# Optimization experiments

Hardware: AMD Instinct MI355X
Metric: run time of the kernel (lower is better)

The kernel has to match this reference:

```python
import jax, jax.numpy as jnp
import numpy as np

# ---- model hyperparameters (match init_kwargs) ----
NUM_INPUT, NUM_HIDDEN, NUM_OUTPUT = 2048, 65536, 512
FAN_OUT = 256
TAU, THRESHOLD = 20.0, 0.3
SPIKE_DELAY = 1  # must be 1 for the one-step-delay scan formulation below
N = NUM_INPUT + NUM_HIDDEN + NUM_OUTPUT
HID_START, OUT_START = NUM_INPUT, NUM_INPUT + NUM_HIDDEN
SURROGATE_SCALE = 25.0


@jax.custom_vjp
def spike(v):
    """Heaviside spike with sigmoid surrogate gradient (SurrogateSpike)."""
    return (v >= THRESHOLD).astype(v.dtype)

def _spike_fwd(v):
    return spike(v), v

def _spike_bwd(v, g):
    s = jax.nn.sigmoid(SURROGATE_SCALE * (v - THRESHOLD))
    return (g * SURROGATE_SCALE * s * (1.0 - s),)

spike.defvjp(_spike_fwd, _spike_bwd)


def make_targets(seed=42):
    """Structured random connectivity (mirrors _generate_random_targets ranges)."""
    rng = np.random.default_rng(seed)
    t = np.empty((N, FAN_OUT), dtype=np.int64)
    # input neurons -> hidden
    t[:NUM_INPUT] = rng.integers(HID_START, OUT_START, size=(NUM_INPUT, FAN_OUT))
    # hidden neurons -> hidden+output, excluding self
    hid = rng.integers(HID_START, N, size=(NUM_HIDDEN, FAN_OUT))
    src = np.arange(HID_START, OUT_START)[:, None]
    R = N - HID_START
    hid = np.where(hid == src, HID_START + (hid - HID_START + 1) % R, hid)
    t[HID_START:OUT_START] = hid
    # output neurons -> hidden
    t[OUT_START:] = rng.integers(HID_START, OUT_START, size=(NUM_OUTPUT, FAN_OUT))
    return jnp.asarray(t, dtype=jnp.int32)


def setup_inputs() -> dict:
    key = jax.random.key(0)
    k1, k2 = jax.random.split(key)
    weights = jax.random.normal(k1, (N, FAN_OUT), dtype=jnp.float32) * 0.3
    input_spikes = jax.random.bernoulli(k2, 0.2, (NUM_INPUT,))
    return {"input_spikes": input_spikes, "weights": weights,
            "targets": make_targets(), "max_timesteps": 50}


def _simulate(input_spikes, weights, targets, max_timesteps):
    decay_base = jnp.exp(jnp.float32(-1.0 / TAU))
    idx = jnp.arange(N)
    flat_targets = targets.reshape(-1)  # [N*FAN_OUT]

    inp = jnp.zeros(N, bool).at[:NUM_INPUT].set(input_spikes)
    pot = jnp.zeros(N, jnp.float32)
    last_update = jnp.zeros(N, jnp.int32)
    has_fired = inp
    strength = jnp.where(inp, 2.0, 0.0).astype(jnp.float32)
    out_times = jnp.full(NUM_OUTPUT, -1, jnp.int32)
    fire_now = inp  # input spikes scheduled on the wheel at t=0

    def step(carry, t):
        pot, last_update, has_fired, strength, fire_now, out_times = carry
        # contributions of spiking sources: spike_strength[src] * weights[src]
        src_val = jnp.where(fire_now, strength, 0.0)                 # [N]
        contrib = (src_val[:, None] * weights).reshape(-1)           # [N*FAN_OUT]
        # neurons that receive at least one spike this step (the 'unique_targets')
        hits = jnp.zeros(N, jnp.float32).at[flat_targets].add(
            jnp.repeat(fire_now.astype(jnp.float32), FAN_OUT))
        is_target = hits > 0
        # lazy retroactive decay only on touched neurons
        dt = (t - last_update).astype(jnp.float32)
        pot = jnp.where(is_target, pot * decay_base ** dt, pot)
        last_update = jnp.where(is_target, t, last_update)
        # scatter-add contributions (zeros for non-firing sources)
        pot = pot.at[flat_targets].add(contrib)
        # spike check with refractory mask
        probs = spike(pot) * (1.0 - has_fired.astype(jnp.float32))
        new_fired = probs > 0.5
        has_fired = has_fired | new_fired
        strength = jnp.where(new_fired, probs, strength)
        out_times = jnp.where(new_fired[OUT_START:] & (out_times < 0), t, out_times)
        # schedule hidden spikes for delivery at t + 1 (spike_delay == 1)
        fire_next = new_fired & (idx < OUT_START)
        # reset membrane of newly fired non-output neurons
        reset = jnp.where(idx >= OUT_START, 0.0, probs)
        pot = pot * (1.0 - reset)
        return (pot, last_update, has_fired, strength, fire_next, out_times), None

    carry = (pot, last_update, has_fired, strength, fire_now, out_times)
    carry, _ = jax.lax.scan(step, carry, jnp.arange(max_timesteps, dtype=jnp.int32))
    pot, last_update, has_fired, strength, _, out_times = carry
    # final decay to end of simulation window
    final_dt = (max_timesteps - last_update).astype(jnp.float32)
    pot = pot * decay_base ** final_dt
    return out_times, pot[OUT_START:]


def reference(input_spikes, weights, targets, max_timesteps):
    out_times, out_pot = _simulate(input_spikes, weights, targets, max_timesteps)
    return out_times, out_pot
```

## Files before the change

kernel.cpp:

```cpp
#include <hip/hip_runtime.h>
#include <math.h>

#define N_TOTAL    68096
#define NUM_INPUT  2048
#define NUM_OUTPUT 512
#define OUT_START  67584
#define N_TGT      66048
#define FAN_OUT    256
#define THRESH     0.3f
#define T_MAX      50
#define T_BIG      12
#define BM_WORDS   2064
#define LIST_CAP   12288

#define HALF_SZ    33024
#define N_CHUNK    128
#define DENSE_THR  2000

__device__ __forceinline__ int calc_chunks(int fcnt) {
    int c = fcnt >> 7;
    if (c < 1) c = 1;
    if (c > N_CHUNK) c = N_CHUNK;
    return c;
}

__global__ __launch_bounds__(256) void init_k(
    const unsigned int* __restrict__ in0,
    float* pot, float* acc, int* last_up, unsigned char* fired,
    int* frontier0, int* cnt, float* out_f, float* decay_tab)
{
    __shared__ int sF, sG;
    const int tid = threadIdx.x;
    if (tid == 0) { sF = 0; sG = 0; }
    __syncthreads();
    for (int k = tid; k < 512; k += 256) {
        unsigned int v = in0[k];
        if (v == 0x3F800000u) atomicAdd(&sF, 1);
        else if (v > 1u)      sG = 1;
    }
    __syncthreads();
    const int mode = (sF >= 8) ? 1 : (sG ? 2 : 0);

    const int i = blockIdx.x * 256 + tid;
    const int lane = tid & 63;
    if (i <= T_MAX) {
        float base = expf(-0.05f);
        decay_tab[i] = (float)pow((double)base, (double)i);
    }
    if (i < NUM_OUTPUT) out_f[i] = -1.0f;
    bool want = false;
    if (i < N_TOTAL) {
        pot[i] = 0.0f;
        acc[i] = 0.0f;
        last_up[i] = 0;
        bool s = false;
        if (i < NUM_INPUT) {
            if (mode == 0)      s = ((const int*)in0)[i] != 0;
            else if (mode == 1) s = ((const float*)in0)[i] != 0.0f;
            else                s = ((const unsigned char*)in0)[i] != 0;
        }
        fired[i] = s ? 1 : 0;
        want = s;
    }
    unsigned long long m = __ballot(want);
    if (m) {
        int leader = __ffsll((long long)m) - 1;
        int base = 0;
        if (lane == leader) base = atomicAdd(&cnt[0], __popcll(m));
        base = __shfl(base, leader, 64);
        if (want) {
            int off = __popcll(m & ((1ull << (unsigned)lane) - 1ull));
            frontier0[base + off] = i;
        }
    }
}

__global__ __launch_bounds__(1024) void step_scatter_k(
    const int* __restrict__ fr, const int* __restrict__ cnt_cur,
    int* cnt_next,
    const int* __restrict__ targets, const float* __restrict__ weights,
    float* __restrict__ acc, float* __restrict__ rep)
{
    __shared__ float lacc[HALF_SZ];
    const int fcnt = *cnt_cur;
    const int tid  = threadIdx.x;
    if (blockIdx.x == 0 && tid == 0) *cnt_next = 0;
    if (fcnt == 0) return;

    if (fcnt < DENSE_THR) {
        const int nq = fcnt * (FAN_OUT / 4);
        const int stride = gridDim.x * 1024;
        for (int q = blockIdx.x * 1024 + tid; q < nq; q += stride) {
            int s  = fr[q >> 6];
            int j4 = (q & 63) << 2;
            const int base = s * FAN_OUT + j4;
            int4   tg = *(const int4*)  (targets + base);
            float4 wv = *(const float4*)(weights + base);
            float  st = (s < NUM_INPUT) ? 2.0f : 1.0f;
            atomicAdd(&acc[tg.x], st * wv.x);
            atomicAdd(&acc[tg.y], st * wv.y);
            atomicAdd(&acc[tg.z], st * wv.z);
            atomicAdd(&acc[tg.w], st * wv.w);
        }
        return;
    }

    const int chunks = calc_chunks(fcnt);
    const int c = blockIdx.x & 127;
    const int h = blockIdx.x >> 7;
    if (c >= chunks) return;
    const int base = NUM_INPUT + h * HALF_SZ;
    for (int k = tid; k < HALF_SZ / 4; k += 1024)
        ((float4*)lacc)[k] = make_float4(0.f, 0.f, 0.f, 0.f);
    __syncthreads();
    const int lo = (int)(((long long)fcnt * c)       / chunks);
    const int hi = (int)(((long long)fcnt * (c + 1)) / chunks);
    const int nq = (hi - lo) << 6;
    for (int q = tid; q < nq; q += 2048) {
        const int q2 = q + 1024;
        const bool hasB = q2 < nq;
        const int sA  = fr[lo + (q >> 6)];
        const int sB  = hasB ? fr[lo + (q2 >> 6)] : sA;
        const int ebA = sA * FAN_OUT + ((q  & 63) << 2);
        const int ebB = sB * FAN_OUT + ((q2 & 63) << 2);
        int4   tgA = *(const int4*)  (targets + ebA);
        float4 wvA = *(const float4*)(weights + ebA);
        int4   tgB = *(const int4*)  (targets + ebB);
        float4 wvB = *(const float4*)(weights + ebB);
        const float stA = (sA < NUM_INPUT) ? 2.0f : 1.0f;
        const float stB = (sB < NUM_INPUT) ? 2.0f : 1.0f;
        int x;
        x = tgA.x - base; if ((unsigned)x < HALF_SZ) atomicAdd(&lacc[x], stA * wvA.x);
        x = tgA.y - base; if ((unsigned)x < HALF_SZ) atomicAdd(&lacc[x], stA * wvA.y);
        x = tgA.z - base; if ((unsigned)x < HALF_SZ) atomicAdd(&lacc[x], stA * wvA.z);
        x = tgA.w - base; if ((unsigned)x < HALF_SZ) atomicAdd(&lacc[x], stA * wvA.w);
        if (hasB) {
            x = tgB.x - base; if ((unsigned)x < HALF_SZ) atomicAdd(&lacc[x], stB * wvB.x);
            x = tgB.y - base; if ((unsigned)x < HALF_SZ) atomicAdd(&lacc[x], stB * wvB.y);
            x = tgB.z - base; if ((unsigned)x < HALF_SZ) atomicAdd(&lacc[x], stB * wvB.z);
            x = tgB.w - base; if ((unsigned)x < HALF_SZ) atomicAdd(&lacc[x], stB * wvB.w);
        }
    }
    __syncthreads();
    float4* out = (float4*)(rep + (size_t)((c << 1) + h) * HALF_SZ);
    for (int k = tid; k < HALF_SZ / 4; k += 1024) out[k] = ((float4*)lacc)[k];
}

__global__ __launch_bounds__(128) void step_update_k(
    const float* __restrict__ rep, const int* __restrict__ cnt_cur,
    float* __restrict__ pot, float* __restrict__ acc,
    int* __restrict__ last_up, unsigned char* __restrict__ fired,
    int* __restrict__ frontier_next, int* __restrict__ cnt_next,
    float* __restrict__ out_f, const float* __restrict__ decay_tab, int t)
{
    const int fcnt = *cnt_cur;
    if (fcnt == 0) return;
    const int g = blockIdx.x * 128 + threadIdx.x;
    const int lane = threadIdx.x & 63;
    bool w2 = false;
    const int n = NUM_INPUT + g;
    {
        float a;
        if (fcnt < DENSE_THR) {
            a = acc[n];
            if (a != 0.0f) acc[n] = 0.0f;
        } else {
            const int chunks = calc_chunks(fcnt);
            const int hh  = (g >= HALF_SZ) ? 1 : 0;
            const int idx = g - hh * HALF_SZ;
            const float* p0 = rep + (size_t)hh * HALF_SZ + idx;
            float a0 = 0.f, a1 = 0.f, a2 = 0.f, a3 = 0.f;
            int c = 0;
            for (; c + 3 < chunks; c += 4) {
                a0 += p0[(size_t)((c + 0) << 1) * HALF_SZ];
                a1 += p0[(size_t)((c + 1) << 1) * HALF_SZ];
                a2 += p0[(size_t)((c + 2) << 1) * HALF_SZ];
                a3 += p0[(size_t)((c + 3) << 1) * HALF_SZ];
            }
            for (; c < chunks; ++c)
                a0 += p0[(size_t)(c << 1) * HALF_SZ];
            a = (a0 + a1) + (a2 + a3);
        }
        if (a != 0.0f) {
            float p = pot[n] * decay_tab[t - last_up[n]] + a;
            last_up[n] = t;
            if (!fired[n] && p >= THRESH) {
                fired[n] = 1;
                if (n < OUT_START) { p = 0.0f; w2 = true; }
                else out_f[n - OUT_START] = (float)t;
            }
            pot[n] = p;
        }
    }
    unsigned long long m = __ballot(w2);
    if (m) {
        int leader = __ffsll((long long)m) - 1;
        int base = 0;
        if (lane == leader) base = atomicAdd(cnt_next, __popcll(m));
        base = __shfl(base, leader, 64);
        if (w2) {
            int off = __popcll(m & ((1ull << (unsigned)lane) - 1ull));
            frontier_next[base + off] = n;
        }
    }
}

__global__ __launch_bounds__(1024) void tail_k(
    float* __restrict__ pot, float* __restrict__ acc,
    int* __restrict__ last_up, unsigned char* __restrict__ fired,
    int* __restrict__ fr0, int* __restrict__ fr1, int* __restrict__ cnt,
    const int* __restrict__ targets, const float* __restrict__ weights,
    float* __restrict__ out_f, const float* __restrict__ decay_tab)
{
    __shared__ unsigned bm[BM_WORDS];
    __shared__ int      lst[LIST_CAP];
    __shared__ int      lcnt, ovf;
    __shared__ float    sdecay[T_MAX + 1];
    const int tid = threadIdx.x;
    if (tid <= T_MAX) sdecay[tid] = decay_tab[tid];

    for (int t = T_BIG; t < T_MAX; ++t) {
        const int cur = t & 1, nxt = cur ^ 1;
        for (int k = tid; k < BM_WORDS; k += 1024) bm[k] = 0u;
        if (tid == 0) { lcnt = 0; ovf = 0; cnt[nxt] = 0; }
        __syncthreads();
        const int fcnt = cnt[cur];
        if (fcnt == 0) break;
        const int* fr  = (cur == 0) ? fr0 : fr1;
        int*       frn = (cur == 0) ? fr1 : fr0;

        const int nq = fcnt * (FAN_OUT / 4);
        for (int q = tid; q < nq; q += 1024) {
            int s  = fr[q >> 6];
            int j4 = (q & 63) << 2;
            const int base = s * FAN_OUT + j4;
            int4   tg = *(const int4*)  (targets + base);
            float4 wv = *(const float4*)(weights + base);
            float  st = (s < NUM_INPUT) ? 2.0f : 1.0f;
            #define EDGE(TG, WV) do {                                         \
                atomicAdd(&acc[TG], st * (WV));                               \
                int b = (TG) - NUM_INPUT;                                     \
                unsigned bit = 1u << (b & 31);                                \
                unsigned old = atomicOr(&bm[b >> 5], bit);                    \
                if (!(old & bit)) {                                           \
                    int p_ = atomicAdd(&lcnt, 1);                             \
                    if (p_ < LIST_CAP) lst[p_] = (TG); else ovf = 1;          \
                } } while (0)
            EDGE(tg.x, wv.x); EDGE(tg.y, wv.y);
            EDGE(tg.z, wv.z); EDGE(tg.w, wv.w);
            #undef EDGE
        }
        __syncthreads();

        const int M = lcnt;
        const bool full = (ovf != 0);
        const int lo = full ? (NUM_INPUT + tid) : tid;
        const int hi = full ? N_TOTAL : M;
        for (int k = lo; k < hi; k += 1024) {
            const int n = full ? k : lst[k];
            float a = __hip_atomic_load(&acc[n], __ATOMIC_RELAXED,
                                        __HIP_MEMORY_SCOPE_AGENT);
            if (a != 0.0f) {
                __hip_atomic_store(&acc[n], 0.0f, __ATOMIC_RELAXED,
                                   __HIP_MEMORY_SCOPE_AGENT);
                float p = pot[n] * sdecay[t - last_up[n]] + a;
                last_up[n] = t;
                if (!fired[n] && p >= THRESH) {
                    fired[n] = 1;
                    if (n < OUT_START) {
                        p = 0.0f;
                        int pos = atomicAdd(&cnt[nxt], 1);
                        frn[pos] = n;
                    } else out_f[n - OUT_START] = (float)t;
                }
                pot[n] = p;
            }
        }
        __syncthreads();
    }

    __syncthreads();
    for (int i = tid; i < NUM_OUTPUT; i += 1024) {
        int n = OUT_START + i;
        out_f[NUM_OUTPUT + i] = pot[n] * sdecay[T_MAX - last_up[n]];
    }
}

extern "C" void kernel_launch(void* const* d_in, const int* in_sizes, int n_in,
                              void* d_out, int out_size, void* d_ws, size_t ws_size,
                              hipStream_t stream) {
    const void*  in_spikes = d_in[0];
    const float* weights   = (const float*)d_in[1];
    const int*   targets   = (const int*)d_in[2];
    float*       out_f     = (float*)d_out;

    char* w = (char*)d_ws;
    int*   cnt       = (int*)w;
    float* decay_tab = (float*)(w + 256);
    float* pot       = (float*)(w + 512);
    float* acc       = pot + N_TOTAL;
    int*   last_up   = (int*)(acc + N_TOTAL);
    int*   fr0       = last_up + N_TOTAL;
    int*   fr1       = fr0 + N_TOTAL;
    unsigned char* fired = (unsigned char*)(fr1 + N_TOTAL);
    size_t base_bytes = (size_t)((char*)(fired + N_TOTAL) - w);
    size_t rep_off    = (base_bytes + 255) & ~(size_t)255;
    float* rep        = (float*)(w + rep_off);

    hipMemsetAsync(cnt, 0, 16, stream);
    init_k<<<266, 256, 0, stream>>>((const unsigned int*)in_spikes,
                                    pot, acc, last_up, fired,
                                    fr0, cnt, out_f, decay_tab);

    int* fr[2] = {fr0, fr1};
    for (int t = 0; t < T_BIG; ++t) {
        const int cur = t & 1, nxt = cur ^ 1;
        step_scatter_k<<<2 * N_CHUNK, 1024, 0, stream>>>(
            fr[cur], &cnt[cur], &cnt[nxt], targets, weights, acc, rep);
        step_update_k<<<516, 128, 0, stream>>>(
            rep, &cnt[cur], pot, acc, last_up, fired,
            fr[nxt], &cnt[nxt], out_f, decay_tab, t);
    }
    tail_k<<<1, 1024, 0, stream>>>(pot, acc, last_up, fired, fr0, fr1, cnt,
                                   targets, weights, out_f, decay_tab);
}
```

Baseline: 320.5 us.

## Skip scatter to already-fired hidden neurons via shared fired bitmask

Keeps a global bitmask of hidden neurons that have already fired and copies it into shared memory in the scatter kernels. Edges whose target already fired are dropped, and the weight load is skipped when all four targets in a vector are dead. The update kernels skip already-fired neurons. It also raises the dense threshold so more steps take the global-atomic path. The trade-offs are extra shared memory and bitmask reads, and the pot/last_up values of fired hidden neurons no longer change, which only matters if those values are observed.

```diff
diff --git a/kernel.cpp b/kernel.cpp
--- a/kernel.cpp
+++ b/kernel.cpp
@@ -6,6 +6,8 @@
 #define NUM_OUTPUT 512
 #define OUT_START  67584
 #define N_TGT      66048
+#define NUM_HIDDEN 65536
+#define FB_WORDS   2048
 #define FAN_OUT    256
 #define THRESH     0.3f
 #define T_MAX      50
@@ -15,7 +17,8 @@
 
 #define HALF_SZ    33024
 #define N_CHUNK    128
-#define DENSE_THR  2000
+#define DENSE_THR  6000
+
 
 __device__ __forceinline__ int calc_chunks(int fcnt) {
     int c = fcnt >> 7;
@@ -27,7 +30,8 @@
 __global__ __launch_bounds__(256) void init_k(
     const unsigned int* __restrict__ in0,
     float* pot, float* acc, int* last_up, unsigned char* fired,
-    int* frontier0, int* cnt, float* out_f, float* decay_tab)
+    int* frontier0, int* cnt, float* out_f, float* decay_tab,
+    unsigned* fbits)
 {
     __shared__ int sF, sG;
     const int tid = threadIdx.x;
@@ -48,6 +52,7 @@
         decay_tab[i] = (float)pow((double)base, (double)i);
     }
     if (i < NUM_OUTPUT) out_f[i] = -1.0f;
+    if (i < FB_WORDS)   fbits[i] = 0u;
     bool want = false;
     if (i < N_TOTAL) {
         pot[i] = 0.0f;
@@ -75,32 +80,44 @@
     }
 }
 
+#define LIVE(SFB, TG) ({ int b_ = (TG) - NUM_INPUT; \
+    (b_ >= NUM_HIDDEN) || !((SFB[b_ >> 5] >> (b_ & 31)) & 1u); })
+
 __global__ __launch_bounds__(1024) void step_scatter_k(
     const int* __restrict__ fr, const int* __restrict__ cnt_cur,
     int* cnt_next,
     const int* __restrict__ targets, const float* __restrict__ weights,
-    float* __restrict__ acc, float* __restrict__ rep)
+    float* __restrict__ acc, float* __restrict__ rep,
+    const unsigned* __restrict__ fbits)
 {
-    __shared__ float lacc[HALF_SZ];
+    __shared__ float    lacc[HALF_SZ];
+    __shared__ unsigned sfb[FB_WORDS];
     const int fcnt = *cnt_cur;
     const int tid  = threadIdx.x;
     if (blockIdx.x == 0 && tid == 0) *cnt_next = 0;
     if (fcnt == 0) return;
 
+    for (int k = tid; k < FB_WORDS; k += 1024) sfb[k] = fbits[k];
+
     if (fcnt < DENSE_THR) {
+        __syncthreads();
         const int nq = fcnt * (FAN_OUT / 4);
         const int stride = gridDim.x * 1024;
         for (int q = blockIdx.x * 1024 + tid; q < nq; q += stride) {
             int s  = fr[q >> 6];
             int j4 = (q & 63) << 2;
             const int base = s * FAN_OUT + j4;
-            int4   tg = *(const int4*)  (targets + base);
-            float4 wv = *(const float4*)(weights + base);
-            float  st = (s < NUM_INPUT) ? 2.0f : 1.0f;
-            atomicAdd(&acc[tg.x], st * wv.x);
-            atomicAdd(&acc[tg.y], st * wv.y);
-            atomicAdd(&acc[tg.z], st * wv.z);
-            atomicAdd(&acc[tg.w], st * wv.w);
+            int4 tg = *(const int4*)(targets + base);
+            const bool lx = LIVE(sfb, tg.x), ly = LIVE(sfb, tg.y);
+            const bool lz = LIVE(sfb, tg.z), lw = LIVE(sfb, tg.w);
+            if (lx | ly | lz | lw) {
+                float4 wv = *(const float4*)(weights + base);
+                float  st = (s < NUM_INPUT) ? 2.0f : 1.0f;
+                if (lx) atomicAdd(&acc[tg.x], st * wv.x);
+                if (ly) atomicAdd(&acc[tg.y], st * wv.y);
+                if (lz) atomicAdd(&acc[tg.z], st * wv.z);
+                if (lw) atomicAdd(&acc[tg.w], st * wv.w);
+            }
         }
         return;
     }
@@ -123,22 +140,36 @@
         const int sB  = hasB ? fr[lo + (q2 >> 6)] : sA;
         const int ebA = sA * FAN_OUT + ((q  & 63) << 2);
         const int ebB = sB * FAN_OUT + ((q2 & 63) << 2);
-        int4   tgA = *(const int4*)  (targets + ebA);
-        float4 wvA = *(const float4*)(weights + ebA);
-        int4   tgB = *(const int4*)  (targets + ebB);
-        float4 wvB = *(const float4*)(weights + ebB);
-        const float stA = (sA < NUM_INPUT) ? 2.0f : 1.0f;
-        const float stB = (sB < NUM_INPUT) ? 2.0f : 1.0f;
+        int4 tgA = *(const int4*)(targets + ebA);
+        int4 tgB = *(const int4*)(targets + ebB);
         int x;
-        x = tgA.x - base; if ((unsigned)x < HALF_SZ) atomicAdd(&lacc[x], stA * wvA.x);
-        x = tgA.y - base; if ((unsigned)x < HALF_SZ) atomicAdd(&lacc[x], stA * wvA.y);
-        x = tgA.z - base; if ((unsigned)x < HALF_SZ) atomicAdd(&lacc[x], stA * wvA.z);
-        x = tgA.w - base; if ((unsigned)x < HALF_SZ) atomicAdd(&lacc[x], stA * wvA.w);
+        {
+            x = tgA.x - base; const bool kx = (unsigned)x < HALF_SZ && LIVE(sfb, tgA.x);
+            int y = tgA.y - base; const bool ky = (unsigned)y < HALF_SZ && LIVE(sfb, tgA.y);
+            int z = tgA.z - base; const bool kz = (unsigned)z < HALF_SZ && LIVE(sfb, tgA.z);
+            int u = tgA.w - base; const bool ku = (unsigned)u < HALF_SZ && LIVE(sfb, tgA.w);
+            if (kx | ky | kz | ku) {
+                float4 wv = *(const float4*)(weights + ebA);
+                const float st = (sA < NUM_INPUT) ? 2.0f : 1.0f;
+                if (kx) atomicAdd(&lacc[x], st * wv.x);
+                if (ky) atomicAdd(&lacc[y], st * wv.y);
+                if (kz) atomicAdd(&lacc[z], st * wv.z);
+                if (ku) atomicAdd(&lacc[u], st * wv.w);
+            }
+        }
         if (hasB) {
-            x = tgB.x - base; if ((unsigned)x < HALF_SZ) atomicAdd(&lacc[x], stB * wvB.x);
-            x = tgB.y - base; if ((unsigned)x < HALF_SZ) atomicAdd(&lacc[x], stB * wvB.y);
-            x = tgB.z - base; if ((unsigned)x < HALF_SZ) atomicAdd(&lacc[x], stB * wvB.z);
-            x = tgB.w - base; if ((unsigned)x < HALF_SZ) atomicAdd(&lacc[x], stB * wvB.w);
+            x = tgB.x - base; const bool kx = (unsigned)x < HALF_SZ && LIVE(sfb, tgB.x);
+            int y = tgB.y - base; const bool ky = (unsigned)y < HALF_SZ && LIVE(sfb, tgB.y);
+            int z = tgB.z - base; const bool kz = (unsigned)z < HALF_SZ && LIVE(sfb, tgB.z);
+            int u = tgB.w - base; const bool ku = (unsigned)u < HALF_SZ && LIVE(sfb, tgB.w);
+            if (kx | ky | kz | ku) {
+                float4 wv = *(const float4*)(weights + ebB);
+                const float st = (sB < NUM_INPUT) ? 2.0f : 1.0f;
+                if (kx) atomicAdd(&lacc[x], st * wv.x);
+                if (ky) atomicAdd(&lacc[y], st * wv.y);
+                if (kz) atomicAdd(&lacc[z], st * wv.z);
+                if (ku) atomicAdd(&lacc[u], st * wv.w);
+            }
         }
     }
     __syncthreads();
@@ -151,7 +182,8 @@
     float* __restrict__ pot, float* __restrict__ acc,
     int* __restrict__ last_up, unsigned char* __restrict__ fired,
     int* __restrict__ frontier_next, int* __restrict__ cnt_next,
-    float* __restrict__ out_f, const float* __restrict__ decay_tab, int t)
+    float* __restrict__ out_f, const float* __restrict__ decay_tab, int t,
+    unsigned* __restrict__ fbits)
 {
     const int fcnt = *cnt_cur;
     if (fcnt == 0) return;
@@ -159,7 +191,7 @@
     const int lane = threadIdx.x & 63;
     bool w2 = false;
     const int n = NUM_INPUT + g;
-    {
+    if (n >= OUT_START || !fired[n]) {
         float a;
         if (fcnt < DENSE_THR) {
             a = acc[n];
@@ -186,8 +218,11 @@
             last_up[n] = t;
             if (!fired[n] && p >= THRESH) {
                 fired[n] = 1;
-                if (n < OUT_START) { p = 0.0f; w2 = true; }
-                else out_f[n - OUT_START] = (float)t;
+                if (n < OUT_START) {
+                    p = 0.0f; w2 = true;
+                    const int b = n - NUM_INPUT;
+                    atomicOr(&fbits[b >> 5], 1u << (b & 31));
+                } else out_f[n - OUT_START] = (float)t;
             }
             pot[n] = p;
         }
@@ -210,14 +245,17 @@
     int* __restrict__ last_up, unsigned char* __restrict__ fired,
     int* __restrict__ fr0, int* __restrict__ fr1, int* __restrict__ cnt,
     const int* __restrict__ targets, const float* __restrict__ weights,
-    float* __restrict__ out_f, const float* __restrict__ decay_tab)
+    float* __restrict__ out_f, const float* __restrict__ decay_tab,
+    const unsigned* __restrict__ fbits)
 {
     __shared__ unsigned bm[BM_WORDS];
+    __shared__ unsigned sfb[FB_WORDS];
     __shared__ int      lst[LIST_CAP];
     __shared__ int      lcnt, ovf;
     __shared__ float    sdecay[T_MAX + 1];
     const int tid = threadIdx.x;
     if (tid <= T_MAX) sdecay[tid] = decay_tab[tid];
+    for (int k = tid; k < FB_WORDS; k += 1024) sfb[k] = fbits[k];
 
     for (int t = T_BIG; t < T_MAX; ++t) {
         const int cur = t & 1, nxt = cur ^ 1;
@@ -234,10 +272,13 @@
             int s  = fr[q >> 6];
             int j4 = (q & 63) << 2;
             const int base = s * FAN_OUT + j4;
-            int4   tg = *(const int4*)  (targets + base);
+            int4 tg = *(const int4*)(targets + base);
+            const bool lx = LIVE(sfb, tg.x), ly = LIVE(sfb, tg.y);
+            const bool lz = LIVE(sfb, tg.z), lw = LIVE(sfb, tg.w);
+            if (!(lx | ly | lz | lw)) continue;
             float4 wv = *(const float4*)(weights + base);
             float  st = (s < NUM_INPUT) ? 2.0f : 1.0f;
-            #define EDGE(TG, WV) do {                                         \
+            #define EDGE(L, TG, WV) if (L) {                                  \
                 atomicAdd(&acc[TG], st * (WV));                               \
                 int b = (TG) - NUM_INPUT;                                     \
                 unsigned bit = 1u << (b & 31);                                \
@@ -245,9 +286,9 @@
                 if (!(old & bit)) {                                           \
                     int p_ = atomicAdd(&lcnt, 1);                             \
                     if (p_ < LIST_CAP) lst[p_] = (TG); else ovf = 1;          \
-                } } while (0)
-            EDGE(tg.x, wv.x); EDGE(tg.y, wv.y);
-            EDGE(tg.z, wv.z); EDGE(tg.w, wv.w);
+                } }
+            EDGE(lx, tg.x, wv.x); EDGE(ly, tg.y, wv.y);
+            EDGE(lz, tg.z, wv.z); EDGE(lw, tg.w, wv.w);
             #undef EDGE
         }
         __syncthreads();
@@ -258,6 +299,7 @@
         const int hi = full ? N_TOTAL : M;
         for (int k = lo; k < hi; k += 1024) {
             const int n = full ? k : lst[k];
+            if (n < OUT_START && fired[n]) continue;
             float a = __hip_atomic_load(&acc[n], __ATOMIC_RELAXED,
                                         __HIP_MEMORY_SCOPE_AGENT);
             if (a != 0.0f) {
@@ -271,6 +313,8 @@
                         p = 0.0f;
                         int pos = atomicAdd(&cnt[nxt], 1);
                         frn[pos] = n;
+                        const int b = n - NUM_INPUT;
+                        atomicOr(&sfb[b >> 5], 1u << (b & 31));
                     } else out_f[n - OUT_START] = (float)t;
                 }
                 pot[n] = p;
@@ -295,14 +339,15 @@
     float*       out_f     = (float*)d_out;
 
     char* w = (char*)d_ws;
-    int*   cnt       = (int*)w;
-    float* decay_tab = (float*)(w + 256);
-    float* pot       = (float*)(w + 512);
-    float* acc       = pot + N_TOTAL;
-    int*   last_up   = (int*)(acc + N_TOTAL);
-    int*   fr0       = last_up + N_TOTAL;
-    int*   fr1       = fr0 + N_TOTAL;
-    unsigned char* fired = (unsigned char*)(fr1 + N_TOTAL);
+    int*      cnt       = (int*)w;
+    float*    decay_tab = (float*)(w + 256);
+    float*    pot       = (float*)(w + 512);
+    float*    acc       = pot + N_TOTAL;
+    int*      last_up   = (int*)(acc + N_TOTAL);
+    int*      fr0       = last_up + N_TOTAL;
+    int*      fr1       = fr0 + N_TOTAL;
+    unsigned* fbits     = (unsigned*)(fr1 + N_TOTAL);
+    unsigned char* fired = (unsigned char*)(fbits + FB_WORDS);
     size_t base_bytes = (size_t)((char*)(fired + N_TOTAL) - w);
     size_t rep_off    = (base_bytes + 255) & ~(size_t)255;
     float* rep        = (float*)(w + rep_off);
@@ -310,17 +355,17 @@
     hipMemsetAsync(cnt, 0, 16, stream);
     init_k<<<266, 256, 0, stream>>>((const unsigned int*)in_spikes,
                                     pot, acc, last_up, fired,
-                                    fr0, cnt, out_f, decay_tab);
+                                    fr0, cnt, out_f, decay_tab, fbits);
 
     int* fr[2] = {fr0, fr1};
     for (int t = 0; t < T_BIG; ++t) {
         const int cur = t & 1, nxt = cur ^ 1;
         step_scatter_k<<<2 * N_CHUNK, 1024, 0, stream>>>(
-            fr[cur], &cnt[cur], &cnt[nxt], targets, weights, acc, rep);
+            fr[cur], &cnt[cur], &cnt[nxt], targets, weights, acc, rep, fbits);
         step_update_k<<<516, 128, 0, stream>>>(
             rep, &cnt[cur], pot, acc, last_up, fired,
-            fr[nxt], &cnt[nxt], out_f, decay_tab, t);
+            fr[nxt], &cnt[nxt], out_f, decay_tab, t, fbits);
     }
     tail_k<<<1, 1024, 0, stream>>>(pot, acc, last_up, fired, fr0, fr1, cnt,
-                                   targets, weights, out_f, decay_tab);
-}
+                                   targets, weights, out_f, decay_tab, fbits);
+}
```

After: 269.4 us. 1.19x faster.
